# Performance work log

Measured on AMD Instinct MI355X. Metric: run time of the kernel, lower is better.

The kernel has to match this reference:

```python
import math
import jax, jax.numpy as jnp
import numpy as np

B, NQ, NK, DIM, H, HD = 2, 1024, 2048, 1024, 16, 64


def setup_inputs() -> dict:
    key = jax.random.key(0)
    ks = jax.random.split(key, 12)
    s = 1.0 / math.sqrt(DIM)
    return {
        "q": jax.random.normal(ks[0], (B, NQ, DIM), jnp.float32),
        "k": jax.random.normal(ks[1], (B, NK, DIM), jnp.float32),
        "v": jax.random.normal(ks[2], (B, NK, DIM), jnp.float32),
        "distances": jax.random.uniform(ks[3], (B, NQ, NK), jnp.float32),
        "attn_mask": jax.random.bernoulli(ks[4], 0.5, (B, NQ, NK)),
        "key_padding_mask_q": jax.random.bernoulli(ks[5], 0.5, (B, NQ)),
        "key_padding_mask_k": jax.random.bernoulli(ks[6], 0.5, (B, NK)),
        "Wq": jax.random.normal(ks[7], (H * HD, DIM), jnp.float32) * s,
        "Wk": jax.random.normal(ks[8], (H * HD, DIM), jnp.float32) * s,
        "Wv": jax.random.normal(ks[9], (H * HD, DIM), jnp.float32) * s,
        "Wo": jax.random.normal(ks[10], (DIM, H * HD), jnp.float32) * s,
        "gate_alpha": jnp.float32(0.1),
    }


def reference(q, k, v, distances, attn_mask, key_padding_mask_q,
              key_padding_mask_k, Wq, Wk, Wv, Wo, gate_alpha):
    bsz, q_len, _ = q.shape
    k_len = k.shape[1]
    neg = jnp.finfo(q.dtype).min

    # projections -> (B, H, N, HD)
    qp = (q @ Wq.T).reshape(bsz, q_len, H, HD).transpose(0, 2, 1, 3)
    kp = (k @ Wk.T).reshape(bsz, k_len, H, HD).transpose(0, 2, 1, 3)
    vp = (v @ Wv.T).reshape(bsz, k_len, H, HD).transpose(0, 2, 1, 3)

    scores = jnp.einsum('bhqd,bhkd->bhqk', qp, kp) / math.sqrt(HD)
    scores = jnp.where(attn_mask[:, None, :, :], scores, neg)
    scores = jnp.where(key_padding_mask_k[:, None, None, :], scores, neg)

    attn = jax.nn.softmax(scores, axis=-1)  # (B,H,NQ,NK)

    # distance gating: mask, batch-mean normalize, exponential gate
    d = distances * attn_mask.astype(distances.dtype)
    d = d * key_padding_mask_k[:, None, :].astype(d.dtype)
    mean = d.sum(axis=(-1, -2)) / (q_len * k_len + 1e-6)
    mean = jnp.maximum(mean, 1e-6)[:, None, None]
    d = d / mean
    alpha = jax.nn.softplus(gate_alpha)
    gate = jnp.exp(-alpha * d)[:, None, :, :]  # (B,1,NQ,NK)

    w = attn * gate
    w = w / (w.sum(axis=-1, keepdims=True) + 1e-6)

    out = jnp.einsum('bhqk,bhkd->bhqd', w, vp)
    out = out.transpose(0, 2, 1, 3).reshape(bsz, q_len, H * HD)
    out = out * key_padding_mask_q[:, :, None].astype(out.dtype)
    return out @ Wo.T
```

## Files before the change

### kernel.cpp

```cpp
#include <hip/hip_runtime.h>
#include <hip/hip_bf16.h>
#include <cfloat>

#define B_   2
#define NQ_  1024
#define NK_  2048
#define H_   16
#define HD_  64
#define VPAD 2176
#define GPAD 2112
#define NSPLIT 2

typedef float  floatx4 __attribute__((ext_vector_type(4)));
typedef __bf16 bf16x8  __attribute__((ext_vector_type(8)));
typedef __bf16 bf16x4  __attribute__((ext_vector_type(4)));

static __device__ __forceinline__ floatx4 mfma16(bf16x8 a, bf16x8 b, floatx4 c) {
    return __builtin_amdgcn_mfma_f32_16x16x32_bf16(a, b, c, 0, 0, 0);
}

static __device__ __forceinline__ void gl_lds(const __bf16* g, __bf16* lbase,
                                              int lane) {
#if __has_builtin(__builtin_amdgcn_global_load_lds)
    __builtin_amdgcn_global_load_lds(
        (const __attribute__((address_space(1))) void*)g,
        (__attribute__((address_space(3))) void*)lbase, 16, 0, 0);
#else
    *(bf16x8*)(lbase + lane * 8) = *(const bf16x8*)g;
#endif
}

struct CvtArgs {
    const float* src[7];
    __bf16*      dst[7];
};

__global__ __launch_bounds__(256) void cvt_mean_kernel(
    CvtArgs a, const float* __restrict__ dist, const int* __restrict__ amask,
    const int* __restrict__ kpmk, float* __restrict__ msum)
{
    if (blockIdx.x >= 7168) {
        const int mb = blockIdx.x - 7168;
        const int b  = mb >> 7;
        const float* d  = dist  + (size_t)b * NQ_ * NK_;
        const int*   am = amask + (size_t)b * NQ_ * NK_;
        const int*   km = kpmk  + b * NK_;
        const int total = NQ_ * NK_ / 4;
        float s = 0.f;
        for (int i = (mb & 127) * 256 + threadIdx.x; i < total; i += 128 * 256) {
            const int idx = i * 4;
            const int kk  = idx & (NK_ - 1);
            float4 dv = *(const float4*)(d + idx);
            int4   mv = *(const int4*)(am + idx);
            int4   kv = *(const int4*)(km + kk);
            s += (mv.x && kv.x) ? dv.x : 0.f;
            s += (mv.y && kv.y) ? dv.y : 0.f;
            s += (mv.z && kv.z) ? dv.z : 0.f;
            s += (mv.w && kv.w) ? dv.w : 0.f;
        }
        #pragma unroll
        for (int off = 32; off >= 1; off >>= 1) s += __shfl_down(s, off);
        __shared__ float wsum[4];
        if ((threadIdx.x & 63) == 0) wsum[threadIdx.x >> 6] = s;
        __syncthreads();
        if (threadIdx.x == 0)
            atomicAdd(&msum[b], wsum[0] + wsum[1] + wsum[2] + wsum[3]);
        return;
    }
    size_t r = (size_t)blockIdx.x * 256 + threadIdx.x;
    int s;
    if (r < 262144)                  { s = 0; }
    else if ((r -= 262144) < 524288) { s = 1; }
    else if ((r -= 524288) < 524288) { s = 2; }
    else { r -= 524288; s = 3 + (int)(r >> 17); r &= 131071; }
    const float* sp = a.src[s] + r * 8;
    float4 f0 = *(const float4*)sp;
    float4 f1 = *(const float4*)(sp + 4);
    bf16x8 o;
    o[0] = (__bf16)f0.x; o[1] = (__bf16)f0.y; o[2] = (__bf16)f0.z; o[3] = (__bf16)f0.w;
    o[4] = (__bf16)f1.x; o[5] = (__bf16)f1.y; o[6] = (__bf16)f1.z; o[7] = (__bf16)f1.w;
    *(bf16x8*)(a.dst[s] + r * 8) = o;
}

__global__ __launch_bounds__(256) void gate_kernel(
    const float* __restrict__ dist, const int* __restrict__ amask,
    const int* __restrict__ kpmk, const float* __restrict__ msum,
    const float* __restrict__ galpha, __bf16* __restrict__ gate)
{
    const int b = blockIdx.y;
    const float mean  = fmaxf(msum[b] / ((float)(NQ_ * NK_) + 1e-6f), 1e-6f);
    const float alpha = log1pf(__expf(galpha[0]));
    const float c     = -alpha / mean;
    const int i  = blockIdx.x * 256 + threadIdx.x;
    const int q  = i >> 9;
    const int k4 = (i & 511) * 4;
    const size_t src = ((size_t)b * NQ_ + q) * NK_ + k4;
    float4 dv = *(const float4*)(dist + src);
    int4   mv = *(const int4*)(amask + src);
    int4   kv = *(const int4*)(kpmk + b * NK_ + k4);
    bf16x4 r;
    r[0] = (mv.x && kv.x) ? (__bf16)__expf(c * dv.x) : (__bf16)0.f;
    r[1] = (mv.y && kv.y) ? (__bf16)__expf(c * dv.y) : (__bf16)0.f;
    r[2] = (mv.z && kv.z) ? (__bf16)__expf(c * dv.z) : (__bf16)0.f;
    r[3] = (mv.w && kv.w) ? (__bf16)__expf(c * dv.w) : (__bf16)0.f;
    *(bf16x4*)&gate[((size_t)b * NQ_ + q) * GPAD + k4] = r;
}

template <typename EPI>
static __device__ __forceinline__ void gemm128_core(
    const __bf16* __restrict__ A, const __bf16* __restrict__ Bw,
    int m0, int n0, __bf16* As, __bf16* Bs, EPI epi)
{
    const int t    = threadIdx.x;
    const int w    = t >> 6, lane = t & 63;
    const int lrow = lane & 15, quad = lane >> 4;
    const int lr   = lane >> 2, lc = lane & 3;

    floatx4 acc[4][4];
    #pragma unroll
    for (int mi = 0; mi < 4; mi++)
        #pragma unroll
        for (int ni = 0; ni < 4; ni++) acc[mi][ni] = floatx4{0.f, 0.f, 0.f, 0.f};

    const __bf16* ga = A  + (size_t)(m0 + w * 32 + lr) * 1024 + lc * 8;
    const __bf16* gb = Bw + (size_t)(n0 + w * 32 + lr) * 1024 + lc * 8;

    for (int k0 = 0; k0 < 1024; k0 += 64) {
        __syncthreads();
        #pragma unroll
        for (int h = 0; h < 2; h++) {
            gl_lds(ga + k0 + h * 32,             &As[h * 4096 + (w * 32) * 32],      lane);
            gl_lds(ga + k0 + h * 32 + 16 * 1024, &As[h * 4096 + (w * 32 + 16) * 32], lane);
            gl_lds(gb + k0 + h * 32,             &Bs[h * 4096 + (w * 32) * 32],      lane);
            gl_lds(gb + k0 + h * 32 + 16 * 1024, &Bs[h * 4096 + (w * 32 + 16) * 32], lane);
        }
        __syncthreads();

        #pragma unroll
        for (int h = 0; h < 2; h++) {
            bf16x8 af[4], bfr[4];
            #pragma unroll
            for (int mi = 0; mi < 4; mi++)
                af[mi] = *(const bf16x8*)
                    &As[h * 4096 + ((w & 1) * 64 + mi * 16 + lrow) * 32 + quad * 8];
            #pragma unroll
            for (int ni = 0; ni < 4; ni++)
                bfr[ni] = *(const bf16x8*)
                    &Bs[h * 4096 + ((w >> 1) * 64 + ni * 16 + lrow) * 32 + quad * 8];
            #pragma unroll
            for (int mi = 0; mi < 4; mi++)
                #pragma unroll
                for (int ni = 0; ni < 4; ni++)
                    acc[mi][ni] = mfma16(af[mi], bfr[ni], acc[mi][ni]);
        }
    }

    #pragma unroll
    for (int mi = 0; mi < 4; mi++)
        #pragma unroll
        for (int ni = 0; ni < 4; ni++)
            #pragma unroll
            for (int r = 0; r < 4; r++) {
                const int m = m0 + (w & 1) * 64 + mi * 16 + quad * 4 + r;
                const int n = n0 + (w >> 1) * 64 + ni * 16 + lrow;
                epi(m, n, acc[mi][ni][r]);
            }
}

template <typename EPI>
static __device__ __forceinline__ void gemm64_core(
    const __bf16* __restrict__ A, const __bf16* __restrict__ Bw,
    int m0, int n0, EPI epi)
{
    __shared__ alignas(16) __bf16 As[2][64 * 32];
    __shared__ alignas(16) __bf16 Bs[2][128 * 32];
    const int t    = threadIdx.x;
    const int w    = t >> 6, lane = t & 63;
    const int lrow = lane & 15, quad = lane >> 4;
    const int lr   = lane >> 2, lc = lane & 3;

    floatx4 acc[4][2];
    #pragma unroll
    for (int mi = 0; mi < 4; mi++)
        #pragma unroll
        for (int ni = 0; ni < 2; ni++) acc[mi][ni] = floatx4{0.f, 0.f, 0.f, 0.f};

    const __bf16* ga = A  + (size_t)(m0 + w * 16 + lr) * 1024 + lc * 8;
    const __bf16* gb = Bw + (size_t)(n0 + w * 32 + lr) * 1024 + lc * 8;

    for (int k0 = 0; k0 < 1024; k0 += 64) {
        __syncthreads();
        #pragma unroll
        for (int h = 0; h < 2; h++) {
            gl_lds(ga + k0 + h * 32,             &As[h][(w * 16) * 32],      lane);
            gl_lds(gb + k0 + h * 32,             &Bs[h][(w * 32) * 32],      lane);
            gl_lds(gb + k0 + h * 32 + 16 * 1024, &Bs[h][(w * 32 + 16) * 32], lane);
        }
        __syncthreads();

        #pragma unroll
        for (int h = 0; h < 2; h++) {
            bf16x8 af[4], bfr[2];
            #pragma unroll
            for (int mi = 0; mi < 4; mi++)
                af[mi] = *(const bf16x8*)
                    &As[h][(mi * 16 + lrow) * 32 + quad * 8];
            #pragma unroll
            for (int ni = 0; ni < 2; ni++)
                bfr[ni] = *(const bf16x8*)
                    &Bs[h][(w * 32 + ni * 16 + lrow) * 32 + quad * 8];
            #pragma unroll
            for (int mi = 0; mi < 4; mi++)
                #pragma unroll
                for (int ni = 0; ni < 2; ni++)
                    acc[mi][ni] = mfma16(af[mi], bfr[ni], acc[mi][ni]);
        }
    }

    #pragma unroll
    for (int mi = 0; mi < 4; mi++)
        #pragma unroll
        for (int ni = 0; ni < 2; ni++)
            #pragma unroll
            for (int r = 0; r < 4; r++) {
                const int m = m0 + mi * 16 + quad * 4 + r;
                const int n = n0 + w * 32 + ni * 16 + lrow;
                epi(m, n, acc[mi][ni][r]);
            }
}

__global__ __launch_bounds__(256) void proj_kernel(
    const __bf16* __restrict__ qb, const __bf16* __restrict__ kb,
    const __bf16* __restrict__ vb, const __bf16* __restrict__ wqb,
    const __bf16* __restrict__ wkb, const __bf16* __restrict__ wvb,
    __bf16* __restrict__ qp, __bf16* __restrict__ kp,
    __bf16* __restrict__ vpT)
{
    __shared__ alignas(16) __bf16 As[2 * 128 * 32];
    __shared__ alignas(16) __bf16 Bs[2 * 128 * 32];
    const int z = blockIdx.z;
    if (z == 0) {
        if ((int)blockIdx.x >= 16) return;
        gemm128_core(qb, wqb, blockIdx.x * 128, blockIdx.y * 128, As, Bs,
                     [&](int m, int n, float v) {
            const int b = m >> 10, q = m & 1023;
            const int h = n >> 6,  d = n & 63;
            qp[(((size_t)(b * 16 + h) * NQ_ + q) << 6) + d] = (__bf16)v;
        });
    } else if (z == 1) {
        gemm128_core(kb, wkb, blockIdx.x * 128, blockIdx.y * 128, As, Bs,
                     [&](int m, int n, float v) {
            const int b = m >> 11, key = m & 2047;
            const int h = n >> 6,  d = n & 63;
            kp[(((size_t)(b * 16 + h) * NK_ + key) << 6) + d] = (__bf16)v;
        });
    } else {
        gemm128_core(wvb, vb, blockIdx.y * 128, blockIdx.x * 128, As, Bs,
                     [&](int m, int n, float v) {
            const int h = m >> 6,  d = m & 63;
            const int b = n >> 11, key = n & 2047;
            vpT[((size_t)(b * 16 + h) * HD_ + d) * VPAD + key] = (__bf16)v;
        });
    }
}

__global__ __launch_bounds__(256) void oproj_kernel(
    const __bf16* __restrict__ A, const __bf16* __restrict__ W,
    float* __restrict__ Cout)
{
    const int m0 = blockIdx.x * 64, n0 = blockIdx.y * 128;
    gemm64_core(A, W, m0, n0, [&](int m, int n, float v) {
        Cout[(size_t)m * 1024 + n] = v;
    });
}

__global__ __launch_bounds__(256, 2) void attn_kernel(
    const __bf16* __restrict__ qp, const __bf16* __restrict__ kp,
    const __bf16* __restrict__ vpT, const __bf16* __restrict__ gate,
    float* __restrict__ Opart, float* __restrict__ Gpart)
{
    __shared__ __bf16 Ks[64 * 72];
    __shared__ __bf16 Vt[64 * 72];
    __shared__ __bf16 Ps[4][32 * 72];
    const int t    = threadIdx.x;
    const int w    = t >> 6, lane = t & 63;
    const int lrow = lane & 15, quad = lane >> 4;
    const int qt   = blockIdx.x;
    const int bh   = blockIdx.y;
    const int sp   = blockIdx.z;
    const int b    = bh >> 4;
    const int q0   = qt * 128 + w * 32;
    const int k0   = sp * (NK_ / NSPLIT);

    bf16x8 qf[2][2];
    #pragma unroll
    for (int qg = 0; qg < 2; qg++) {
        const __bf16* qb = qp + ((size_t)bh * NQ_ + q0 + qg * 16 + lrow) * HD_ +
                           quad * 8;
        qf[qg][0] = *(const bf16x8*)qb;
        qf[qg][1] = *(const bf16x8*)(qb + 32);
    }

    const int srow0 = t >> 3,        sc0 = t & 7;
    const int srow1 = 32 + (t >> 3), sc1 = t & 7;
    const __bf16* Kg = kp  + (size_t)bh * NK_ * HD_;
    const __bf16* Vg = vpT + (size_t)bh * HD_ * VPAD;
    __bf16* KsW0 = &Ks[srow0 * 72 + sc0 * 8];
    __bf16* KsW1 = &Ks[srow1 * 72 + sc1 * 8];
    __bf16* VtW0 = &Vt[srow0 * 72 + sc0 * 8];
    __bf16* VtW1 = &Vt[srow1 * 72 + sc1 * 8];

    const __bf16* grow[2];
    #pragma unroll
    for (int qg = 0; qg < 2; qg++)
        grow[qg] = gate + ((size_t)b * NQ_ + q0 + qg * 16 + lrow) * GPAD;

    float G[2] = {0.f, 0.f};
    floatx4 O[2][4];
    #pragma unroll
    for (int qg = 0; qg < 2; qg++)
        #pragma unroll
        for (int nb = 0; nb < 4; nb++) O[qg][nb] = floatx4{0.f, 0.f, 0.f, 0.f};

    bf16x8 kr0, kr1, vr0, vr1;
    bf16x4 gr[2][4];
    auto loadt = [&](int kb) {
        kr0 = *(const bf16x8*)(Kg + (size_t)(kb + srow0) * HD_ + sc0 * 8);
        kr1 = *(const bf16x8*)(Kg + (size_t)(kb + srow1) * HD_ + sc1 * 8);
        vr0 = *(const bf16x8*)(Vg + (size_t)srow0 * VPAD + kb + sc0 * 8);
        vr1 = *(const bf16x8*)(Vg + (size_t)srow1 * VPAD + kb + sc1 * 8);
        #pragma unroll
        for (int qg = 0; qg < 2; qg++)
            #pragma unroll
            for (int c = 0; c < 4; c++)
                gr[qg][c] = *(const bf16x4*)(grow[qg] + kb + c * 16 + quad * 4);
    };
    loadt(k0);

    for (int kb = k0; kb < k0 + NK_ / NSPLIT; kb += 64) {
        __syncthreads();
        *(bf16x8*)KsW0 = kr0;
        *(bf16x8*)KsW1 = kr1;
        *(bf16x8*)VtW0 = vr0;
        *(bf16x8*)VtW1 = vr1;
        __syncthreads();

        bf16x4 gcur[2][4];
        #pragma unroll
        for (int qg = 0; qg < 2; qg++)
            #pragma unroll
            for (int c = 0; c < 4; c++) gcur[qg][c] = gr[qg][c];
        if (kb + 64 < k0 + NK_ / NSPLIT) loadt(kb + 64);

        bf16x8 kf0[4], kf1[4];
        #pragma unroll
        for (int c = 0; c < 4; c++) {
            kf0[c] = *(const bf16x8*)&Ks[(c * 16 + lrow) * 72 + quad * 8];
            kf1[c] = *(const bf16x8*)&Ks[(c * 16 + lrow) * 72 + 32 + quad * 8];
        }
        floatx4 s4[2][4];
        #pragma unroll
        for (int qg = 0; qg < 2; qg++)
            #pragma unroll
            for (int c = 0; c < 4; c++) {
                floatx4 a = floatx4{0.f, 0.f, 0.f, 0.f};
                a = mfma16(kf0[c], qf[qg][0], a);
                a = mfma16(kf1[c], qf[qg][1], a);
                s4[qg][c] = a;
            }

        #pragma unroll
        for (int qg = 0; qg < 2; qg++) {
            #pragma unroll
            for (int c = 0; c < 4; c++) {
                const float e0 = __expf(s4[qg][c][0] * 0.125f) * (float)gcur[qg][c][0];
                const float e1 = __expf(s4[qg][c][1] * 0.125f) * (float)gcur[qg][c][1];
                const float e2 = __expf(s4[qg][c][2] * 0.125f) * (float)gcur[qg][c][2];
                const float e3 = __expf(s4[qg][c][3] * 0.125f) * (float)gcur[qg][c][3];
                G[qg] += (e0 + e1) + (e2 + e3);
                bf16x4 pk;
                pk[0] = (__bf16)e0; pk[1] = (__bf16)e1;
                pk[2] = (__bf16)e2; pk[3] = (__bf16)e3;
                *(bf16x4*)&Ps[w][(qg * 16 + lrow) * 72 + c * 16 + quad * 4] = pk;
            }
        }

        bf16x8 pf[2][2];
        #pragma unroll
        for (int qg = 0; qg < 2; qg++)
            #pragma unroll
            for (int tt = 0; tt < 2; tt++)
                pf[qg][tt] = *(const bf16x8*)
                    &Ps[w][(qg * 16 + lrow) * 72 + tt * 32 + quad * 8];
        #pragma unroll
        for (int tt = 0; tt < 2; tt++)
            #pragma unroll
            for (int nb = 0; nb < 4; nb++) {
                bf16x8 vf = *(const bf16x8*)
                    &Vt[(nb * 16 + lrow) * 72 + tt * 32 + quad * 8];
                #pragma unroll
                for (int qg = 0; qg < 2; qg++)
                    O[qg][nb] = mfma16(pf[qg][tt], vf, O[qg][nb]);
            }
    }

    #pragma unroll
    for (int qg = 0; qg < 2; qg++) {
        G[qg] += __shfl_xor(G[qg], 16);
        G[qg] += __shfl_xor(G[qg], 32);
    }
    float* Ob = Opart + ((size_t)(sp * 32 + bh) * NQ_ + q0) * HD_;
    #pragma unroll
    for (int qg = 0; qg < 2; qg++)
        #pragma unroll
        for (int nb = 0; nb < 4; nb++)
            #pragma unroll
            for (int r = 0; r < 4; r++)
                Ob[(size_t)(qg * 16 + quad * 4 + r) * HD_ + nb * 16 + lrow] =
                    O[qg][nb][r];
    if (quad == 0) {
        #pragma unroll
        for (int qg = 0; qg < 2; qg++)
            Gpart[(size_t)(sp * 32 + bh) * NQ_ + q0 + qg * 16 + lrow] = G[qg];
    }
}

__global__ __launch_bounds__(256) void combine_kernel(
    const float* __restrict__ Opart, const float* __restrict__ Gpart,
    const int* __restrict__ kpmq, __bf16* __restrict__ attnout)
{
    const int t  = blockIdx.x * 256 + threadIdx.x;
    const int d4 = (t & 15) * 4;
    const int q  = (t >> 4) & 1023;
    const int bh = t >> 14;
    const int b  = bh >> 4, h = bh & 15;
    float4 o = float4{0.f, 0.f, 0.f, 0.f};
    float  g = 0.f;
    #pragma unroll
    for (int j = 0; j < NSPLIT; j++) {
        float4 oj = *(const float4*)
            (Opart + ((size_t)(j * 32 + bh) * NQ_ + q) * HD_ + d4);
        o.x += oj.x; o.y += oj.y; o.z += oj.z; o.w += oj.w;
        g += Gpart[(size_t)(j * 32 + bh) * NQ_ + q];
    }
    const float f = kpmq[b * NQ_ + q] ? 1.f / (g + 1e-30f) : 0.f;
    bf16x4 r;
    r[0] = (__bf16)(o.x * f);
    r[1] = (__bf16)(o.y * f);
    r[2] = (__bf16)(o.z * f);
    r[3] = (__bf16)(o.w * f);
    *(bf16x4*)&attnout[((size_t)b * NQ_ + q) * 1024 + h * HD_ + d4] = r;
}

extern "C" void kernel_launch(void* const* d_in, const int* in_sizes, int n_in,
                              void* d_out, int out_size, void* d_ws,
                              size_t ws_size, hipStream_t stream)
{
    const float* q      = (const float*)d_in[0];
    const float* k      = (const float*)d_in[1];
    const float* v      = (const float*)d_in[2];
    const float* dist   = (const float*)d_in[3];
    const int*   amask  = (const int*)d_in[4];
    const int*   kpmq   = (const int*)d_in[5];
    const int*   kpmk   = (const int*)d_in[6];
    const float* Wq     = (const float*)d_in[7];
    const float* Wk     = (const float*)d_in[8];
    const float* Wv     = (const float*)d_in[9];
    const float* Wo     = (const float*)d_in[10];
    const float* galpha = (const float*)d_in[11];

    char* p = (char*)d_ws;
    float*  msum = (float*)p;                 p += 256;
    __bf16* qb   = (__bf16*)p;                p += (size_t)2097152 * 2;
    __bf16* kb   = (__bf16*)p;                p += (size_t)4194304 * 2;
    __bf16* vb   = (__bf16*)p;                p += (size_t)4194304 * 2;
    __bf16* wqb  = (__bf16*)p;                p += (size_t)1048576 * 2;
    __bf16* wkb  = (__bf16*)p;                p += (size_t)1048576 * 2;
    __bf16* wvb  = (__bf16*)p;                p += (size_t)1048576 * 2;
    __bf16* wob  = (__bf16*)p;                p += (size_t)1048576 * 2;
    __bf16* qp   = (__bf16*)p;                p += (size_t)2097152 * 2;
    __bf16* kpb  = (__bf16*)p;                p += (size_t)4194304 * 2;
    __bf16* vpT  = (__bf16*)p;                p += (size_t)32 * 64 * VPAD * 2;
    __bf16* gate = (__bf16*)p;                p += (size_t)2048 * GPAD * 2;
    __bf16* attnout = (__bf16*)p;             p += (size_t)2097152 * 2;
    float*  Opart   = (float*)p;              p += (size_t)NSPLIT * 2097152 * 4;
    float*  Gpart   = (float*)p;              p += (size_t)NSPLIT * 32768 * 4;

    CvtArgs ca;
    ca.src[0] = q;  ca.src[1] = k;  ca.src[2] = v;
    ca.src[3] = Wq; ca.src[4] = Wk; ca.src[5] = Wv; ca.src[6] = Wo;
    ca.dst[0] = qb;  ca.dst[1] = kb;  ca.dst[2] = vb;
    ca.dst[3] = wqb; ca.dst[4] = wkb; ca.dst[5] = wvb; ca.dst[6] = wob;

    hipMemsetAsync(msum, 0, 256, stream);
    cvt_mean_kernel<<<7424, 256, 0, stream>>>(ca, dist, amask, kpmk, msum);
    gate_kernel<<<dim3(2048, 2), 256, 0, stream>>>(dist, amask, kpmk, msum,
                                                   galpha, gate);
    proj_kernel<<<dim3(32, 8, 3), 256, 0, stream>>>(qb, kb, vb, wqb, wkb, wvb,
                                                    qp, kpb, vpT);
    attn_kernel<<<dim3(8, 32, NSPLIT), 256, 0, stream>>>(qp, kpb, vpT, gate,
                                                         Opart, Gpart);
    combine_kernel<<<2048, 256, 0, stream>>>(Opart, Gpart, kpmq, attnout);
    oproj_kernel<<<dim3(32, 8), 256, 0, stream>>>(attnout, wob, (float*)d_out);
}
```

Baseline: 255.6 us.

## Fuse gate computation into attention and software-pipeline the PV MFMA stage

The mean-reduction pass now also writes a masked bf16 copy of the distances, with a huge sentinel for masked entries, and the separate gate kernel is removed. The attention kernel folds the exponential gate into the softmax exponent as exp(s/8 + c*d), so the gate costs no extra exp or multiply. Vt and the P staging buffers are double-buffered so the P·V MFMAs of the previous tile overlap with the score computation of the current tile. This drops one full pass over the distance and mask tensors and one launch, in exchange for more LDS, which may lower occupancy.

```diff
diff --git a/kernel.cpp b/kernel.cpp
--- a/kernel.cpp
+++ b/kernel.cpp
@@ -37,7 +37,8 @@
 
 __global__ __launch_bounds__(256) void cvt_mean_kernel(
     CvtArgs a, const float* __restrict__ dist, const int* __restrict__ amask,
-    const int* __restrict__ kpmk, float* __restrict__ msum)
+    const int* __restrict__ kpmk, float* __restrict__ msum,
+    __bf16* __restrict__ dmask)
 {
     if (blockIdx.x >= 7168) {
         const int mb = blockIdx.x - 7168;
@@ -45,18 +46,22 @@
         const float* d  = dist  + (size_t)b * NQ_ * NK_;
         const int*   am = amask + (size_t)b * NQ_ * NK_;
         const int*   km = kpmk  + b * NK_;
+        __bf16*      dm = dmask + (size_t)b * NQ_ * GPAD;
         const int total = NQ_ * NK_ / 4;
         float s = 0.f;
         for (int i = (mb & 127) * 256 + threadIdx.x; i < total; i += 128 * 256) {
             const int idx = i * 4;
             const int kk  = idx & (NK_ - 1);
+            const int q   = i >> 9;
             float4 dv = *(const float4*)(d + idx);
             int4   mv = *(const int4*)(am + idx);
             int4   kv = *(const int4*)(km + kk);
-            s += (mv.x && kv.x) ? dv.x : 0.f;
-            s += (mv.y && kv.y) ? dv.y : 0.f;
-            s += (mv.z && kv.z) ? dv.z : 0.f;
-            s += (mv.w && kv.w) ? dv.w : 0.f;
+            bf16x4 o;
+            if (mv.x && kv.x) { s += dv.x; o[0] = (__bf16)dv.x; } else o[0] = (__bf16)3e38f;
+            if (mv.y && kv.y) { s += dv.y; o[1] = (__bf16)dv.y; } else o[1] = (__bf16)3e38f;
+            if (mv.z && kv.z) { s += dv.z; o[2] = (__bf16)dv.z; } else o[2] = (__bf16)3e38f;
+            if (mv.w && kv.w) { s += dv.w; o[3] = (__bf16)dv.w; } else o[3] = (__bf16)3e38f;
+            *(bf16x4*)&dm[(size_t)q * GPAD + kk] = o;
         }
         #pragma unroll
         for (int off = 32; off >= 1; off >>= 1) s += __shfl_down(s, off);
@@ -80,30 +85,6 @@
     o[0] = (__bf16)f0.x; o[1] = (__bf16)f0.y; o[2] = (__bf16)f0.z; o[3] = (__bf16)f0.w;
     o[4] = (__bf16)f1.x; o[5] = (__bf16)f1.y; o[6] = (__bf16)f1.z; o[7] = (__bf16)f1.w;
     *(bf16x8*)(a.dst[s] + r * 8) = o;
-}
-
-__global__ __launch_bounds__(256) void gate_kernel(
-    const float* __restrict__ dist, const int* __restrict__ amask,
-    const int* __restrict__ kpmk, const float* __restrict__ msum,
-    const float* __restrict__ galpha, __bf16* __restrict__ gate)
-{
-    const int b = blockIdx.y;
-    const float mean  = fmaxf(msum[b] / ((float)(NQ_ * NK_) + 1e-6f), 1e-6f);
-    const float alpha = log1pf(__expf(galpha[0]));
-    const float c     = -alpha / mean;
-    const int i  = blockIdx.x * 256 + threadIdx.x;
-    const int q  = i >> 9;
-    const int k4 = (i & 511) * 4;
-    const size_t src = ((size_t)b * NQ_ + q) * NK_ + k4;
-    float4 dv = *(const float4*)(dist + src);
-    int4   mv = *(const int4*)(amask + src);
-    int4   kv = *(const int4*)(kpmk + b * NK_ + k4);
-    bf16x4 r;
-    r[0] = (mv.x && kv.x) ? (__bf16)__expf(c * dv.x) : (__bf16)0.f;
-    r[1] = (mv.y && kv.y) ? (__bf16)__expf(c * dv.y) : (__bf16)0.f;
-    r[2] = (mv.z && kv.z) ? (__bf16)__expf(c * dv.z) : (__bf16)0.f;
-    r[3] = (mv.w && kv.w) ? (__bf16)__expf(c * dv.w) : (__bf16)0.f;
-    *(bf16x4*)&gate[((size_t)b * NQ_ + q) * GPAD + k4] = r;
 }
 
 template <typename EPI>
@@ -276,12 +257,13 @@
 
 __global__ __launch_bounds__(256, 2) void attn_kernel(
     const __bf16* __restrict__ qp, const __bf16* __restrict__ kp,
-    const __bf16* __restrict__ vpT, const __bf16* __restrict__ gate,
+    const __bf16* __restrict__ vpT, const __bf16* __restrict__ dmask,
+    const float* __restrict__ msum, const float* __restrict__ galpha,
     float* __restrict__ Opart, float* __restrict__ Gpart)
 {
     __shared__ __bf16 Ks[64 * 72];
-    __shared__ __bf16 Vt[64 * 72];
-    __shared__ __bf16 Ps[4][32 * 72];
+    __shared__ __bf16 Vt[2][64 * 72];
+    __shared__ __bf16 Ps[4][2][32 * 72];
     const int t    = threadIdx.x;
     const int w    = t >> 6, lane = t & 63;
     const int lrow = lane & 15, quad = lane >> 4;
@@ -291,6 +273,11 @@
     const int b    = bh >> 4;
     const int q0   = qt * 128 + w * 32;
     const int k0   = sp * (NK_ / NSPLIT);
+    const int NT   = (NK_ / NSPLIT) / 64;
+
+    const float mean  = fmaxf(msum[b] / ((float)(NQ_ * NK_) + 1e-6f), 1e-6f);
+    const float alpha = log1pf(__expf(galpha[0]));
+    const float cg    = -alpha / mean;
 
     bf16x8 qf[2][2];
     #pragma unroll
@@ -303,17 +290,15 @@
 
     const int srow0 = t >> 3,        sc0 = t & 7;
     const int srow1 = 32 + (t >> 3), sc1 = t & 7;
+    const int so0 = srow0 * 72 + sc0 * 8;
+    const int so1 = srow1 * 72 + sc1 * 8;
     const __bf16* Kg = kp  + (size_t)bh * NK_ * HD_;
     const __bf16* Vg = vpT + (size_t)bh * HD_ * VPAD;
-    __bf16* KsW0 = &Ks[srow0 * 72 + sc0 * 8];
-    __bf16* KsW1 = &Ks[srow1 * 72 + sc1 * 8];
-    __bf16* VtW0 = &Vt[srow0 * 72 + sc0 * 8];
-    __bf16* VtW1 = &Vt[srow1 * 72 + sc1 * 8];
 
     const __bf16* grow[2];
     #pragma unroll
     for (int qg = 0; qg < 2; qg++)
-        grow[qg] = gate + ((size_t)b * NQ_ + q0 + qg * 16 + lrow) * GPAD;
+        grow[qg] = dmask + ((size_t)b * NQ_ + q0 + qg * 16 + lrow) * GPAD;
 
     float G[2] = {0.f, 0.f};
     floatx4 O[2][4];
@@ -337,12 +322,15 @@
     };
     loadt(k0);
 
-    for (int kb = k0; kb < k0 + NK_ / NSPLIT; kb += 64) {
-        __syncthreads();
-        *(bf16x8*)KsW0 = kr0;
-        *(bf16x8*)KsW1 = kr1;
-        *(bf16x8*)VtW0 = vr0;
-        *(bf16x8*)VtW1 = vr1;
+    for (int ib = 0; ib < NT; ib++) {
+        const int kb  = k0 + ib * 64;
+        const int cur = ib & 1;
+
+        __syncthreads();
+        *(bf16x8*)&Ks[so0]      = kr0;
+        *(bf16x8*)&Ks[so1]      = kr1;
+        *(bf16x8*)&Vt[cur][so0] = vr0;
+        *(bf16x8*)&Vt[cur][so1] = vr1;
         __syncthreads();
 
         bf16x4 gcur[2][4];
@@ -350,7 +338,7 @@
         for (int qg = 0; qg < 2; qg++)
             #pragma unroll
             for (int c = 0; c < 4; c++) gcur[qg][c] = gr[qg][c];
-        if (kb + 64 < k0 + NK_ / NSPLIT) loadt(kb + 64);
+        if (ib + 1 < NT) loadt(kb + 64);
 
         bf16x8 kf0[4], kf1[4];
         #pragma unroll
@@ -369,35 +357,59 @@
                 s4[qg][c] = a;
             }
 
+        if (ib > 0) {
+            const int prv = cur ^ 1;
+            bf16x8 pf[2][2];
+            #pragma unroll
+            for (int qg = 0; qg < 2; qg++)
+                #pragma unroll
+                for (int tt = 0; tt < 2; tt++)
+                    pf[qg][tt] = *(const bf16x8*)
+                        &Ps[w][prv][(qg * 16 + lrow) * 72 + tt * 32 + quad * 8];
+            #pragma unroll
+            for (int tt = 0; tt < 2; tt++)
+                #pragma unroll
+                for (int nb = 0; nb < 4; nb++) {
+                    bf16x8 vf = *(const bf16x8*)
+                        &Vt[prv][(nb * 16 + lrow) * 72 + tt * 32 + quad * 8];
+                    #pragma unroll
+                    for (int qg = 0; qg < 2; qg++)
+                        O[qg][nb] = mfma16(pf[qg][tt], vf, O[qg][nb]);
+                }
+        }
+
         #pragma unroll
         for (int qg = 0; qg < 2; qg++) {
             #pragma unroll
             for (int c = 0; c < 4; c++) {
-                const float e0 = __expf(s4[qg][c][0] * 0.125f) * (float)gcur[qg][c][0];
-                const float e1 = __expf(s4[qg][c][1] * 0.125f) * (float)gcur[qg][c][1];
-                const float e2 = __expf(s4[qg][c][2] * 0.125f) * (float)gcur[qg][c][2];
-                const float e3 = __expf(s4[qg][c][3] * 0.125f) * (float)gcur[qg][c][3];
+                const float e0 = __expf(fmaf(s4[qg][c][0], 0.125f, cg * (float)gcur[qg][c][0]));
+                const float e1 = __expf(fmaf(s4[qg][c][1], 0.125f, cg * (float)gcur[qg][c][1]));
+                const float e2 = __expf(fmaf(s4[qg][c][2], 0.125f, cg * (float)gcur[qg][c][2]));
+                const float e3 = __expf(fmaf(s4[qg][c][3], 0.125f, cg * (float)gcur[qg][c][3]));
                 G[qg] += (e0 + e1) + (e2 + e3);
                 bf16x4 pk;
                 pk[0] = (__bf16)e0; pk[1] = (__bf16)e1;
                 pk[2] = (__bf16)e2; pk[3] = (__bf16)e3;
-                *(bf16x4*)&Ps[w][(qg * 16 + lrow) * 72 + c * 16 + quad * 4] = pk;
+                *(bf16x4*)&Ps[w][cur][(qg * 16 + lrow) * 72 + c * 16 + quad * 4] = pk;
             }
         }
-
+    }
+
+    {
+        const int prv = (NT - 1) & 1;
         bf16x8 pf[2][2];
         #pragma unroll
         for (int qg = 0; qg < 2; qg++)
             #pragma unroll
             for (int tt = 0; tt < 2; tt++)
                 pf[qg][tt] = *(const bf16x8*)
-                    &Ps[w][(qg * 16 + lrow) * 72 + tt * 32 + quad * 8];
+                    &Ps[w][prv][(qg * 16 + lrow) * 72 + tt * 32 + quad * 8];
         #pragma unroll
         for (int tt = 0; tt < 2; tt++)
             #pragma unroll
             for (int nb = 0; nb < 4; nb++) {
                 bf16x8 vf = *(const bf16x8*)
-                    &Vt[(nb * 16 + lrow) * 72 + tt * 32 + quad * 8];
+                    &Vt[prv][(nb * 16 + lrow) * 72 + tt * 32 + quad * 8];
                 #pragma unroll
                 for (int qg = 0; qg < 2; qg++)
                     O[qg][nb] = mfma16(pf[qg][tt], vf, O[qg][nb]);
@@ -481,7 +493,7 @@
     __bf16* qp   = (__bf16*)p;                p += (size_t)2097152 * 2;
     __bf16* kpb  = (__bf16*)p;                p += (size_t)4194304 * 2;
     __bf16* vpT  = (__bf16*)p;                p += (size_t)32 * 64 * VPAD * 2;
-    __bf16* gate = (__bf16*)p;                p += (size_t)2048 * GPAD * 2;
+    __bf16* dmask = (__bf16*)p;               p += (size_t)2048 * GPAD * 2;
     __bf16* attnout = (__bf16*)p;             p += (size_t)2097152 * 2;
     float*  Opart   = (float*)p;              p += (size_t)NSPLIT * 2097152 * 4;
     float*  Gpart   = (float*)p;              p += (size_t)NSPLIT * 32768 * 4;
@@ -493,12 +505,12 @@
     ca.dst[3] = wqb; ca.dst[4] = wkb; ca.dst[5] = wvb; ca.dst[6] = wob;
 
     hipMemsetAsync(msum, 0, 256, stream);
-    cvt_mean_kernel<<<7424, 256, 0, stream>>>(ca, dist, amask, kpmk, msum);
-    gate_kernel<<<dim3(2048, 2), 256, 0, stream>>>(dist, amask, kpmk, msum,
-                                                   galpha, gate);
+    cvt_mean_kernel<<<7424, 256, 0, stream>>>(ca, dist, amask, kpmk, msum,
+                                              dmask);
     proj_kernel<<<dim3(32, 8, 3), 256, 0, stream>>>(qb, kb, vb, wqb, wkb, wvb,
                                                     qp, kpb, vpT);
-    attn_kernel<<<dim3(8, 32, NSPLIT), 256, 0, stream>>>(qp, kpb, vpT, gate,
+    attn_kernel<<<dim3(8, 32, NSPLIT), 256, 0, stream>>>(qp, kpb, vpT, dmask,
+                                                         msum, galpha,
                                                          Opart, Gpart);
     combine_kernel<<<2048, 256, 0, stream>>>(Opart, Gpart, kpmq, attnout);
     oproj_kernel<<<dim3(32, 8), 256, 0, stream>>>(attnout, wob, (float*)d_out);
```

After: 258.6 us. Within noise of the previous version (+1.2%).
